# Kernel optimization log

Hardware: AMD Instinct MI355X
Metric: run time of the kernel (lower is better)

The kernel has to match this reference:

```python
import jax, jax.numpy as jnp
import numpy as np

HAD_BLOCK = 128
HAD_SCALE = 2.0 ** (-3.5)  # 1/sqrt(128), orthonormal block Hadamard


def _hadamard_matrix(n):
    H = np.array([[1.0]], dtype=np.float32)
    while H.shape[0] < n:
        H = np.block([[H, H], [H, -H]])
    return jnp.asarray(H)

_H = _hadamard_matrix(HAD_BLOCK)


def hadamard_transform(x, scale):
    # x: (..., D) with D % 128 == 0; blockwise Hadamard rotation on last dim
    shp = x.shape
    xb = x.reshape(shp[:-1] + (shp[-1] // HAD_BLOCK, HAD_BLOCK))
    y = jnp.einsum('...b,cb->...c', xb, _H) * scale
    return y.reshape(shp)


def setup_inputs() -> dict:
    key = jax.random.key(0)
    kx, kw, kb = jax.random.split(key, 3)
    B, S, IN, OUT = 4, 2048, 4096, 4096
    x = jax.random.normal(kx, (B, S, IN), dtype=jnp.float32)
    # master fp weight, then preprocess: Hadamard-rotate rows, quantize to int4,
    # pack two nibbles per element (per-out-channel scale/add)
    w = jax.random.normal(kw, (OUT, IN), dtype=jnp.float32) / np.float32(np.sqrt(IN))
    w_had = hadamard_transform(w, HAD_SCALE)
    wmin = w_had.min(axis=1, keepdims=True)
    wmax = w_had.max(axis=1, keepdims=True)
    w_scale = jnp.maximum((wmax - wmin) / 15.0, 1e-8)  # [OUT,1]
    w_add = wmin                                        # [OUT,1]
    w_int = jnp.clip(jnp.round((w_had - w_add) / w_scale), 0, 15).astype(jnp.int32)
    w_int_packed = (w_int[:, ::2] | (w_int[:, 1::2] << 4)).astype(jnp.int32)  # [OUT, IN//2]
    bias = jax.random.normal(kb, (OUT,), dtype=jnp.float32) * 0.01
    return {"x": x, "w_int_packed": w_int_packed, "w_scale": w_scale,
            "w_add": w_add, "bias": bias}


def reference(x, w_int_packed, w_scale, w_add, bias):
    OUT = w_int_packed.shape[0]
    IN = w_int_packed.shape[1] * 2
    # unpack int4 nibbles -> [OUT, IN]
    low = w_int_packed & 0xF
    high = (w_int_packed >> 4) & 0xF
    w_int = jnp.stack([low, high], axis=-1).reshape(OUT, IN).astype(w_scale.dtype)
    # per-out-channel dequant
    w_deq = w_int * w_scale + w_add  # [OUT, IN]
    # fused Hadamard rotation on activations (matches rotated weight)
    a = hadamard_transform(x, HAD_SCALE)  # [B,S,IN]
    y = jnp.einsum('bsi,oi->bso', a, w_deq)
    return y + bias
```

## Files before the change

kernel.cpp:

```cpp
#include <hip/hip_runtime.h>
#include <hip/hip_bf16.h>
#include <hip/hip_fp16.h>

#define IN_DIM 4096
#define OUT_DIM 4096
#define HAD_SCALE_F 0.08838834764831845f

typedef int   i32x4 __attribute__((ext_vector_type(4)));
typedef float f32x4 __attribute__((ext_vector_type(4)));

__global__ __launch_bounds__(256)
void had_rows_q(const float* __restrict__ x, int* __restrict__ aq,
                float* __restrict__ rowsum, float* __restrict__ srow)
{
    __shared__ float wmx[4];
    __shared__ int   wqs[4];
    const int tid = threadIdx.x;
    const int wv  = tid >> 6;
    const size_t row = blockIdx.x;
    const float* xr = x + row * IN_DIM + tid * 16;

    float e[16];
    #pragma unroll
    for (int v = 0; v < 4; ++v) {
        const float4 f = ((const float4*)xr)[v];
        e[v*4+0] = f.x; e[v*4+1] = f.y; e[v*4+2] = f.z; e[v*4+3] = f.w;
    }

    #pragma unroll
    for (int s = 1; s < 16; s <<= 1) {
        #pragma unroll
        for (int i = 0; i < 16; ++i) {
            if (!(i & s)) {
                const float u = e[i], w2 = e[i | s];
                e[i]     = u + w2;
                e[i | s] = u - w2;
            }
        }
    }
    #pragma unroll
    for (int m = 1; m <= 4; m <<= 1) {
        const float sgn = (tid & m) ? -1.0f : 1.0f;
        #pragma unroll
        for (int i = 0; i < 16; ++i) {
            const float p = __shfl_xor(e[i], m, 64);
            e[i] = fmaf(sgn, e[i], p);
        }
    }

    float smax = 0.f;
    #pragma unroll
    for (int i = 0; i < 16; ++i) {
        e[i] *= HAD_SCALE_F;
        smax = fmaxf(smax, fabsf(e[i]));
    }
    #pragma unroll
    for (int off = 32; off > 0; off >>= 1)
        smax = fmaxf(smax, __shfl_xor(smax, off, 64));
    if ((tid & 63) == 0) wmx[wv] = smax;
    __syncthreads();
    const float mx  = fmaxf(fmaxf(wmx[0], wmx[1]), fmaxf(wmx[2], wmx[3]));
    const float inv = (mx > 0.f) ? 127.0f / mx : 0.f;
    const float sa  = mx * (1.0f / 127.0f);

    int qsum = 0;
    int pk[4];
    #pragma unroll
    for (int g2 = 0; g2 < 4; ++g2) {
        const int q0 = (int)rintf(e[g2*4+0] * inv);
        const int q1 = (int)rintf(e[g2*4+1] * inv);
        const int q2 = (int)rintf(e[g2*4+2] * inv);
        const int q3 = (int)rintf(e[g2*4+3] * inv);
        qsum += (q0 + q1) + (q2 + q3);
        pk[g2] = (q0 & 0xFF) | ((q1 & 0xFF) << 8) | ((q2 & 0xFF) << 16) | (q3 << 24);
    }
    *(int4*)&aq[row * (IN_DIM / 4) + tid * 4] = make_int4(pk[0], pk[1], pk[2], pk[3]);

    #pragma unroll
    for (int off = 32; off > 0; off >>= 1) qsum += __shfl_xor(qsum, off, 64);
    if ((tid & 63) == 0) wqs[wv] = qsum;
    __syncthreads();
    if (tid == 0) {
        rowsum[row] = sa * (float)((wqs[0] + wqs[1]) + (wqs[2] + wqs[3]));
        srow[row]   = sa;
    }
}

__global__ __launch_bounds__(256)
void unpack_w4i(const int* __restrict__ wp, unsigned char* __restrict__ wf4)
{
    const int gid = blockIdx.x * 256 + threadIdx.x;
    const int c   = gid & 3;
    const int kt  = (gid >> 2) & 31;
    const int n   = gid >> 7;
    const int kbase = kt * 128 + c * 16;
    const int* row = wp + (size_t)n * (IN_DIM / 2) + (kbase >> 1);
    const int4 plo0 = *(const int4*)(row);
    const int4 plo1 = *(const int4*)(row + 4);
    const int4 phi0 = *(const int4*)(row + 32);
    const int4 phi1 = *(const int4*)(row + 36);

    #define MKD(lo, hi, lo2, hi2) \
        ( (unsigned)(((lo) & 15) | (((hi) & 15) << 4)) \
        | ((unsigned)((((lo) >> 4) & 15) | ((((hi) >> 4) & 15) << 4)) << 8) \
        | ((unsigned)(((lo2) & 15) | (((hi2) & 15) << 4)) << 16) \
        | ((unsigned)((((lo2) >> 4) & 15) | ((((hi2) >> 4) & 15) << 4)) << 24) )

    uint4 o;
    o.x = MKD(plo0.x, phi0.x, plo0.y, phi0.y);
    o.y = MKD(plo0.z, phi0.z, plo0.w, phi0.w);
    o.z = MKD(plo1.x, phi1.x, plo1.y, phi1.y);
    o.w = MKD(plo1.z, phi1.z, plo1.w, phi1.w);
    #undef MKD
    *(uint4*)(wf4 + (size_t)gid * 16) = o;
}

#define NT 32

#define BAR()        asm volatile("s_barrier" ::: "memory")
#define WAIT_VM(N)   asm volatile("s_waitcnt vmcnt(" #N ")" ::: "memory")
#define WAIT_LGKM0() asm volatile("s_waitcnt lgkmcnt(0)" ::: "memory")

#define STAGE_A(buf, kt) do { \
    _Pragma("unroll") for (int R = 0; R < 4; ++R) \
        __builtin_amdgcn_global_load_lds( \
            (const __attribute__((address_space(1))) void*)(sA + ((size_t)R << 17) + (((kt) & 31) << 7)), \
            (__attribute__((address_space(3))) void*)(smem + (buf) * 16384 + R * 4096 + wv * 1024), 16, 0, 0); \
    } while (0)
#define STAGE_B(kt) do { \
    _Pragma("unroll") for (int R = 0; R < 4; ++R) \
        __builtin_amdgcn_global_load_lds( \
            (const __attribute__((address_space(1))) void*)(sB + ((size_t)R << 17) + (((kt) & 31) << 6)), \
            (__attribute__((address_space(3))) void*)(smem + 32768 + R * 4096 + wv * 1024), 16, 0, 0); \
    } while (0)

__global__ __launch_bounds__(256, 2)
void gemm_i8(const signed char* __restrict__ Aq, const unsigned char* __restrict__ Bw4,
             const float* __restrict__ wscale, const float* __restrict__ wadd,
             const float* __restrict__ bias, const float* __restrict__ rowsum,
             const float* __restrict__ srow, float* __restrict__ out)
{
    __shared__ char smem[49152];

    const int tid  = threadIdx.x;
    const int lane = tid & 63;
    const int wv   = tid >> 6;

    const int bid = blockIdx.x;
    const int wg  = (bid & 7) * 128 + (bid >> 3);
    const int m0  = (wg >> 4) * 128;
    const int n0  = (wg & 15) * 256;

    const int art = tid >> 3;
    const int act = (tid & 7) ^ (art & 7);
    const signed char* sA = Aq + (size_t)(m0 + art) * IN_DIM + act * 16;

    const int brt = tid >> 2;
    const int bct = (tid & 3) ^ (brt & 3);
    const unsigned char* sB = Bw4 + (size_t)(n0 + brt) * 2048 + bct * 16;

    const int l15 = lane & 15, g = lane >> 4, l7 = lane & 7, l3 = lane & 3;
    const int aOff = l15 * 128 + ((g ^ l7) << 4);
    const int bOff = 32768 + (wv * 64 + l15) * 64 + ((g ^ l3) << 4);

    i32x4 afr[4][2], b0[4], b1[4];
    i32x4 acc[8][4] = {};

    STAGE_A(0, 0);
    STAGE_B(0);
    WAIT_VM(0);
    BAR();

    #pragma unroll 1
    for (int kt = 0; kt < NT; ++kt) {
        const int cur = kt & 1;

        STAGE_A(cur ^ 1, kt + 1);

        i32x4 bp[4];
        #pragma unroll
        for (int ni = 0; ni < 4; ++ni)
            bp[ni] = *(const i32x4*)(smem + bOff + ni * 1024);
        #pragma unroll
        for (int mi = 0; mi < 4; ++mi) {
            afr[mi][0] = *(const i32x4*)(smem + cur * 16384 + mi * 2048 + aOff);
            afr[mi][1] = *(const i32x4*)(smem + cur * 16384 + mi * 2048 + (aOff ^ 64));
        }
        #pragma unroll
        for (int ni = 0; ni < 4; ++ni) {
            #pragma unroll
            for (int d = 0; d < 4; ++d) {
                b0[ni][d] = bp[ni][d] & 0x0F0F0F0F;
                b1[ni][d] = (int)(((unsigned)bp[ni][d] >> 4) & 0x0F0F0F0F);
            }
        }

        WAIT_LGKM0();
        BAR();
        STAGE_B(kt + 1);

        __builtin_amdgcn_s_setprio(1);
        #pragma unroll
        for (int mi = 0; mi < 4; ++mi)
            #pragma unroll
            for (int ni = 0; ni < 4; ++ni)
                acc[mi][ni] = __builtin_amdgcn_mfma_i32_16x16x64_i8(
                    afr[mi][0], b0[ni], acc[mi][ni], 0, 0, 0);
        #pragma unroll
        for (int mi = 0; mi < 4; ++mi)
            #pragma unroll
            for (int ni = 0; ni < 4; ++ni)
                acc[mi][ni] = __builtin_amdgcn_mfma_i32_16x16x64_i8(
                    afr[mi][1], b1[ni], acc[mi][ni], 0, 0, 0);
        __builtin_amdgcn_s_setprio(0);

        #pragma unroll
        for (int mi = 0; mi < 4; ++mi) {
            afr[mi][0] = *(const i32x4*)(smem + cur * 16384 + (mi + 4) * 2048 + aOff);
            afr[mi][1] = *(const i32x4*)(smem + cur * 16384 + (mi + 4) * 2048 + (aOff ^ 64));
        }
        __builtin_amdgcn_s_setprio(1);
        #pragma unroll
        for (int mi = 0; mi < 4; ++mi)
            #pragma unroll
            for (int ni = 0; ni < 4; ++ni)
                acc[mi + 4][ni] = __builtin_amdgcn_mfma_i32_16x16x64_i8(
                    afr[mi][0], b0[ni], acc[mi + 4][ni], 0, 0, 0);
        #pragma unroll
        for (int mi = 0; mi < 4; ++mi)
            #pragma unroll
            for (int ni = 0; ni < 4; ++ni)
                acc[mi + 4][ni] = __builtin_amdgcn_mfma_i32_16x16x64_i8(
                    afr[mi][1], b1[ni], acc[mi + 4][ni], 0, 0, 0);
        __builtin_amdgcn_s_setprio(0);

        WAIT_VM(0);
        BAR();
    }

    #pragma unroll
    for (int ni = 0; ni < 4; ++ni) {
        const int col = n0 + wv * 64 + ni * 16 + l15;
        const float sc = wscale[col];
        const float ad = wadd[col];
        const float bi = bias[col];
        #pragma unroll
        for (int mi = 0; mi < 8; ++mi) {
            const int row = m0 + mi * 16 + g * 4;
            const float4 rs4 = *(const float4*)&rowsum[row];
            const float4 sr4 = *(const float4*)&srow[row];
            #pragma unroll
            for (int j = 0; j < 4; ++j) {
                const float rs = (j == 0) ? rs4.x : (j == 1) ? rs4.y : (j == 2) ? rs4.z : rs4.w;
                const float sr = (j == 0) ? sr4.x : (j == 1) ? sr4.y : (j == 2) ? sr4.z : sr4.w;
                out[(size_t)(row + j) * OUT_DIM + col] =
                    (float)acc[mi][ni][j] * (sc * sr) + ad * rs + bi;
            }
        }
    }
}

extern "C" void kernel_launch(void* const* d_in, const int* in_sizes, int n_in,
                              void* d_out, int out_size, void* d_ws, size_t ws_size,
                              hipStream_t stream)
{
    const float* x      = (const float*)d_in[0];
    const int*   wp     = (const int*)d_in[1];
    const float* wscale = (const float*)d_in[2];
    const float* wadd   = (const float*)d_in[3];
    const float* bias   = (const float*)d_in[4];
    float*       out    = (float*)d_out;

    const int M = in_sizes[0] / IN_DIM;

    char* ws = (char*)d_ws;
    unsigned char* wf4 = (unsigned char*)ws;
    const size_t wf_bytes = (size_t)OUT_DIM * IN_DIM / 2;
    int* aq = (int*)(ws + wf_bytes);
    const size_t aq_bytes = (size_t)M * IN_DIM;
    float* rowsum = (float*)(ws + wf_bytes + aq_bytes);
    float* srow   = (float*)(ws + wf_bytes + aq_bytes + (size_t)M * 4);

    unpack_w4i<<<(OUT_DIM * 32 * 4) / 256, 256, 0, stream>>>(wp, wf4);

    had_rows_q<<<M, 256, 0, stream>>>(x, aq, rowsum, srow);

    gemm_i8<<<(M / 128) * (OUT_DIM / 256), 256, 0, stream>>>(
        (const signed char*)aq, wf4, wscale, wadd, bias, rowsum, srow, out);
}
```

Baseline: 175.0 us.

## Double-buffer B tile and split waves into a 2x2 grid over the tile

The weight (B) tile now gets its own double buffer in LDS, so its next stage is issued alongside A at the top of each iteration. This removes the mid-iteration lgkmcnt wait and extra barrier that were needed when B had a single buffer. Waves move from each covering all 128 rows by 64 columns to a 2x2 layout of 64 rows by 128 columns. Each wave therefore loads half as many A fragments and twice as many B fragments, and its nibble unpack work doubles. LDS use grows to 64KB per block, which could limit two blocks per CU, and more B registers are live at once.

```diff
diff --git a/kernel.cpp b/kernel.cpp
--- a/kernel.cpp
+++ b/kernel.cpp
@@ -119,7 +119,6 @@
 
 #define BAR()        asm volatile("s_barrier" ::: "memory")
 #define WAIT_VM(N)   asm volatile("s_waitcnt vmcnt(" #N ")" ::: "memory")
-#define WAIT_LGKM0() asm volatile("s_waitcnt lgkmcnt(0)" ::: "memory")
 
 #define STAGE_A(buf, kt) do { \
     _Pragma("unroll") for (int R = 0; R < 4; ++R) \
@@ -127,11 +126,11 @@
             (const __attribute__((address_space(1))) void*)(sA + ((size_t)R << 17) + (((kt) & 31) << 7)), \
             (__attribute__((address_space(3))) void*)(smem + (buf) * 16384 + R * 4096 + wv * 1024), 16, 0, 0); \
     } while (0)
-#define STAGE_B(kt) do { \
+#define STAGE_B(buf, kt) do { \
     _Pragma("unroll") for (int R = 0; R < 4; ++R) \
         __builtin_amdgcn_global_load_lds( \
             (const __attribute__((address_space(1))) void*)(sB + ((size_t)R << 17) + (((kt) & 31) << 6)), \
-            (__attribute__((address_space(3))) void*)(smem + 32768 + R * 4096 + wv * 1024), 16, 0, 0); \
+            (__attribute__((address_space(3))) void*)(smem + 32768 + (buf) * 16384 + R * 4096 + wv * 1024), 16, 0, 0); \
     } while (0)
 
 __global__ __launch_bounds__(256, 2)
@@ -140,11 +139,13 @@
              const float* __restrict__ bias, const float* __restrict__ rowsum,
              const float* __restrict__ srow, float* __restrict__ out)
 {
-    __shared__ char smem[49152];
+    __shared__ char smem[65536];
 
     const int tid  = threadIdx.x;
     const int lane = tid & 63;
     const int wv   = tid >> 6;
+    const int wm   = wv >> 1;
+    const int wn   = wv & 1;
 
     const int bid = blockIdx.x;
     const int wg  = (bid & 7) * 128 + (bid >> 3);
@@ -160,14 +161,14 @@
     const unsigned char* sB = Bw4 + (size_t)(n0 + brt) * 2048 + bct * 16;
 
     const int l15 = lane & 15, g = lane >> 4, l7 = lane & 7, l3 = lane & 3;
-    const int aOff = l15 * 128 + ((g ^ l7) << 4);
-    const int bOff = 32768 + (wv * 64 + l15) * 64 + ((g ^ l3) << 4);
-
-    i32x4 afr[4][2], b0[4], b1[4];
-    i32x4 acc[8][4] = {};
+    const int aOff = (wm * 64 + l15) * 128 + ((g ^ l7) << 4);
+    const int bOff = (wn * 128 + l15) * 64 + ((g ^ l3) << 4);
+
+    i32x4 afr[4][2], b0[8], b1[8];
+    i32x4 acc[4][8] = {};
 
     STAGE_A(0, 0);
-    STAGE_B(0);
+    STAGE_B(0, 0);
     WAIT_VM(0);
     BAR();
 
@@ -176,77 +177,68 @@
         const int cur = kt & 1;
 
         STAGE_A(cur ^ 1, kt + 1);
-
-        i32x4 bp[4];
-        #pragma unroll
-        for (int ni = 0; ni < 4; ++ni)
-            bp[ni] = *(const i32x4*)(smem + bOff + ni * 1024);
+        STAGE_B(cur ^ 1, kt + 1);
+
+        {
+            i32x4 bp[4];
+            #pragma unroll
+            for (int ni = 0; ni < 4; ++ni)
+                bp[ni] = *(const i32x4*)(smem + 32768 + cur * 16384 + bOff + ni * 1024);
+            #pragma unroll
+            for (int ni = 0; ni < 4; ++ni)
+                #pragma unroll
+                for (int d = 0; d < 4; ++d) {
+                    b0[ni][d] = bp[ni][d] & 0x0F0F0F0F;
+                    b1[ni][d] = (int)(((unsigned)bp[ni][d] >> 4) & 0x0F0F0F0F);
+                }
+        }
+        {
+            i32x4 bp[4];
+            #pragma unroll
+            for (int ni = 0; ni < 4; ++ni)
+                bp[ni] = *(const i32x4*)(smem + 32768 + cur * 16384 + bOff + (ni + 4) * 1024);
+            #pragma unroll
+            for (int ni = 0; ni < 4; ++ni)
+                #pragma unroll
+                for (int d = 0; d < 4; ++d) {
+                    b0[ni + 4][d] = bp[ni][d] & 0x0F0F0F0F;
+                    b1[ni + 4][d] = (int)(((unsigned)bp[ni][d] >> 4) & 0x0F0F0F0F);
+                }
+        }
         #pragma unroll
         for (int mi = 0; mi < 4; ++mi) {
             afr[mi][0] = *(const i32x4*)(smem + cur * 16384 + mi * 2048 + aOff);
             afr[mi][1] = *(const i32x4*)(smem + cur * 16384 + mi * 2048 + (aOff ^ 64));
         }
-        #pragma unroll
-        for (int ni = 0; ni < 4; ++ni) {
-            #pragma unroll
-            for (int d = 0; d < 4; ++d) {
-                b0[ni][d] = bp[ni][d] & 0x0F0F0F0F;
-                b1[ni][d] = (int)(((unsigned)bp[ni][d] >> 4) & 0x0F0F0F0F);
-            }
-        }
-
-        WAIT_LGKM0();
-        BAR();
-        STAGE_B(kt + 1);
 
         __builtin_amdgcn_s_setprio(1);
         #pragma unroll
         for (int mi = 0; mi < 4; ++mi)
             #pragma unroll
-            for (int ni = 0; ni < 4; ++ni)
+            for (int ni = 0; ni < 8; ++ni)
                 acc[mi][ni] = __builtin_amdgcn_mfma_i32_16x16x64_i8(
                     afr[mi][0], b0[ni], acc[mi][ni], 0, 0, 0);
         #pragma unroll
         for (int mi = 0; mi < 4; ++mi)
             #pragma unroll
-            for (int ni = 0; ni < 4; ++ni)
+            for (int ni = 0; ni < 8; ++ni)
                 acc[mi][ni] = __builtin_amdgcn_mfma_i32_16x16x64_i8(
                     afr[mi][1], b1[ni], acc[mi][ni], 0, 0, 0);
         __builtin_amdgcn_s_setprio(0);
 
-        #pragma unroll
-        for (int mi = 0; mi < 4; ++mi) {
-            afr[mi][0] = *(const i32x4*)(smem + cur * 16384 + (mi + 4) * 2048 + aOff);
-            afr[mi][1] = *(const i32x4*)(smem + cur * 16384 + (mi + 4) * 2048 + (aOff ^ 64));
-        }
-        __builtin_amdgcn_s_setprio(1);
-        #pragma unroll
-        for (int mi = 0; mi < 4; ++mi)
-            #pragma unroll
-            for (int ni = 0; ni < 4; ++ni)
-                acc[mi + 4][ni] = __builtin_amdgcn_mfma_i32_16x16x64_i8(
-                    afr[mi][0], b0[ni], acc[mi + 4][ni], 0, 0, 0);
-        #pragma unroll
-        for (int mi = 0; mi < 4; ++mi)
-            #pragma unroll
-            for (int ni = 0; ni < 4; ++ni)
-                acc[mi + 4][ni] = __builtin_amdgcn_mfma_i32_16x16x64_i8(
-                    afr[mi][1], b1[ni], acc[mi + 4][ni], 0, 0, 0);
-        __builtin_amdgcn_s_setprio(0);
-
         WAIT_VM(0);
         BAR();
     }
 
     #pragma unroll
-    for (int ni = 0; ni < 4; ++ni) {
-        const int col = n0 + wv * 64 + ni * 16 + l15;
+    for (int ni = 0; ni < 8; ++ni) {
+        const int col = n0 + wn * 128 + ni * 16 + l15;
         const float sc = wscale[col];
         const float ad = wadd[col];
         const float bi = bias[col];
         #pragma unroll
-        for (int mi = 0; mi < 8; ++mi) {
-            const int row = m0 + mi * 16 + g * 4;
+        for (int mi = 0; mi < 4; ++mi) {
+            const int row = m0 + wm * 64 + mi * 16 + g * 4;
             const float4 rs4 = *(const float4*)&rowsum[row];
             const float4 sr4 = *(const float4*)&srow[row];
             #pragma unroll
```

Measured after the change: 171.5 us. -2.0%, faster.
